# Performance work log

Measured on AMD Instinct MI355X. Metric: run time of the kernel, lower is better.

The kernel has to match this reference:

```python
import jax, jax.numpy as jnp
import numpy as np

EPS = 1e-6

def setup_inputs() -> dict:
    key = jax.random.key(0)
    S, U, D = 512, 32, 512
    dvecs = jax.random.normal(key, (S, U, D), dtype=jnp.float32)
    w = jnp.array([10.0], dtype=jnp.float32)
    b = jnp.array([-5.0], dtype=jnp.float32)
    return {"dvecs": dvecs, "w": w, "b": b}


def _ge2e_loss(dvecs, w, b):
    S, U, D = dvecs.shape
    # Full centroids [S, D]
    centroids = dvecs.mean(axis=1)
    # Leave-one-out centroids [S, U, D] (equivalent to the roll/unfold/mean trick)
    loo = (dvecs.sum(axis=1, keepdims=True) - dvecs) / (U - 1)
    # Norms, clamped like F.cosine_similarity eps
    dn = jnp.linalg.norm(dvecs, axis=-1)        # [S, U]
    cn = jnp.linalg.norm(centroids, axis=-1)    # [S]
    ln = jnp.linalg.norm(loo, axis=-1)          # [S, U]
    # Cosine sim of every utterance vs every speaker centroid: [S, U, S]
    sim_all = jnp.einsum('sud,jd->suj', dvecs, centroids) / jnp.maximum(dn[..., None] * cn[None, None, :], EPS)
    # Self-speaker column uses the leave-one-out centroid (index_copy in torch code)
    sim_self = jnp.einsum('sud,sud->su', dvecs, loo) / jnp.maximum(dn * ln, EPS)
    spk = jnp.arange(S)
    self_mask = spk[:, None, None] == spk[None, None, :]          # [S, 1, S] -> broadcasts to [S, U, S]
    sim = jnp.where(self_mask, sim_self[..., None], sim_all)
    logits = sim * w[0] + b[0]
    losses = -jax.nn.log_softmax(logits, axis=2)                  # [S, U, S]
    # Select losses[s, u, s] and sum (index_select of diagonal entries)
    return jnp.sum(jnp.where(self_mask, losses, 0.0))


def reference(dvecs, w, b):
    return _ge2e_loss(dvecs, w, b)
```

## Files before the change

### kernel.cpp

```cpp
#include <hip/hip_runtime.h>
#include <math.h>

#define NS 512
#define NU 32
#define ND 512
#define GEPS 1e-6f

typedef float f4 __attribute__((ext_vector_type(4)));
typedef _Float16 half8 __attribute__((ext_vector_type(8)));


__global__ __launch_bounds__(256) void prep_full(const float* __restrict__ dvecs,
                                                 _Float16* __restrict__ bpk,
                                                 float* __restrict__ cn2,
                                                 float* __restrict__ dn2,
                                                 _Float16* __restrict__ apk) {
    const int s = blockIdx.x, t = threadIdx.x;
    const int l = t & 63, wv = t >> 6, l15 = l & 15, lg = l >> 4;
    const float* base = dvecs + (size_t)s * NU * ND;
    __shared__ float red[4];

    const int d0 = t * 2;
    float sx = 0.f, sy = 0.f;
    #pragma unroll 4
    for (int u = 0; u < NU; ++u) {
        float2 v = *(const float2*)(base + u * ND + d0);
        sx += v.x; sy += v.y;
    }
    sx *= (1.0f / NU); sy *= (1.0f / NU);
    float c2 = sx * sx + sy * sy;
    #pragma unroll
    for (int m = 1; m < 64; m <<= 1) c2 += __shfl_xor(c2, m);
    if ((t & 63) == 0) red[t >> 6] = c2;

    {
        _Float16 hx = (_Float16)sx, hy = (_Float16)sy;
        _Float16 lx = (_Float16)(sx - (float)hx), ly = (_Float16)(sy - (float)hy);
        const int ct_g = s >> 4, cl15 = s & 15;
        const int tt = d0 >> 5, blg = (d0 >> 3) & 3, j = d0 & 7;
        size_t hbase = ((size_t)(ct_g * 16 + tt)) * 1024 + (blg * 16 + cl15) * 8 + j;
        unsigned hi2 = (unsigned)__builtin_bit_cast(unsigned short, hx)
                     | ((unsigned)__builtin_bit_cast(unsigned short, hy) << 16);
        unsigned lo2 = (unsigned)__builtin_bit_cast(unsigned short, lx)
                     | ((unsigned)__builtin_bit_cast(unsigned short, ly) << 16);
        *(unsigned*)(bpk + hbase)       = hi2;
        *(unsigned*)(bpk + hbase + 512) = lo2;
    }
    __syncthreads();
    if (t == 0) cn2[s] = red[0] + red[1] + red[2] + red[3];

    {
        const int u = t >> 3, jj = t & 7;
        const float* up = base + u * ND + jj * 4;
        float q = 0.f;
        #pragma unroll
        for (int i = 0; i < 16; ++i) {
            f4 v = *(const f4*)(up + i * 32);
            q += v[0]*v[0] + v[1]*v[1] + v[2]*v[2] + v[3]*v[3];
        }
        q += __shfl_xor(q, 1); q += __shfl_xor(q, 2); q += __shfl_xor(q, 4);
        if (jj == 0) dn2[s * NU + u] = q;
    }

    #pragma unroll
    for (int i = 0; i < 8; ++i) {
        const int idx = wv * 8 + i;
        const int rt = idx >> 4, tk = idx & 15;
        const int u = rt * 16 + l15, k = tk * 32 + lg * 8;
        const float* ap = base + (size_t)u * ND + k;
        f4 a0 = *(const f4*)ap;
        f4 a1 = *(const f4*)(ap + 4);
        half8 h, lo;
        #pragma unroll
        for (int i2 = 0; i2 < 4; ++i2) {
            _Float16 h0 = (_Float16)a0[i2];
            h[i2]     = h0; lo[i2]     = (_Float16)(a0[i2] - (float)h0);
            _Float16 h1 = (_Float16)a1[i2];
            h[4 + i2] = h1; lo[4 + i2] = (_Float16)(a1[i2] - (float)h1);
        }
        _Float16* cb = apk + ((size_t)(s * 2 + rt) * 16 + tk) * 1024 + l * 8;
        *(half8*)cb         = h;
        *(half8*)(cb + 512) = lo;
    }
}

__global__ __launch_bounds__(512, 4) void ge2e_full(const _Float16* __restrict__ apk,
                                                    const _Float16* __restrict__ bpk,
                                                    const float* __restrict__ cn2,
                                                    const float* __restrict__ dn2,
                                                    const float* __restrict__ wp,
                                                    const float* __restrict__ bp,
                                                    float* __restrict__ out) {
    const int s = blockIdx.x, tid = threadIdx.x;
    const int l = tid & 63, wv = tid >> 6;
    const int l15 = l & 15, lg = l >> 4;

    f4 acc[2][4];
    #pragma unroll
    for (int rt = 0; rt < 2; ++rt)
        #pragma unroll
        for (int ct = 0; ct < 4; ++ct) acc[rt][ct] = (f4){0.f, 0.f, 0.f, 0.f};

    const _Float16* Ab = apk + (size_t)s * 32 * 1024 + l * 8;
    const _Float16* Bb = bpk + (size_t)(wv * 4) * 16 * 1024 + l * 8;

    for (int t = 0; t < 16; ++t) {
        half8 bh[4], bl[4], ah[2], al[2];
        #pragma unroll
        for (int ct = 0; ct < 4; ++ct) {
            const _Float16* p = Bb + (size_t)(ct * 16 + t) * 1024;
            bh[ct] = *(const half8*)p;
            bl[ct] = *(const half8*)(p + 512);
        }
        #pragma unroll
        for (int rt = 0; rt < 2; ++rt) {
            const _Float16* p = Ab + (size_t)(rt * 16 + t) * 1024;
            ah[rt] = *(const half8*)p;
            al[rt] = *(const half8*)(p + 512);
        }
        #pragma unroll
        for (int ct = 0; ct < 4; ++ct)
            #pragma unroll
            for (int rt = 0; rt < 2; ++rt) {
                acc[rt][ct] = __builtin_amdgcn_mfma_f32_16x16x32_f16(ah[rt], bh[ct], acc[rt][ct], 0, 0, 0);
                acc[rt][ct] = __builtin_amdgcn_mfma_f32_16x16x32_f16(ah[rt], bl[ct], acc[rt][ct], 0, 0, 0);
                acc[rt][ct] = __builtin_amdgcn_mfma_f32_16x16x32_f16(al[rt], bh[ct], acc[rt][ct], 0, 0, 0);
                acc[rt][ct] = __builtin_amdgcn_mfma_f32_16x16x32_f16(al[rt], bl[ct], acc[rt][ct], 0, 0, 0);
            }
    }

    __shared__ float sDn2[32], sSelf[32], sMax[8][32], sSum[8][32], sRow[32];
    if (tid < 32) sDn2[tid] = dn2[s * NU + tid];
    __syncthreads();

    const float w = wp[0], bb = bp[0];
    const float cn2s = cn2[s];
    float dv[2][4];
    #pragma unroll
    for (int rt = 0; rt < 2; ++rt)
        #pragma unroll
        for (int r = 0; r < 4; ++r) dv[rt][r] = sDn2[rt * 16 + lg * 4 + r];

    const bool owner = (wv == (s >> 6)) && (l15 == (s & 15));
    const int  ctd   = (s >> 4) & 3;

    float dotc[2][4];
    #pragma unroll
    for (int ct = 0; ct < 4; ++ct)
        if (ct == ctd)
            #pragma unroll
            for (int rt = 0; rt < 2; ++rt)
                #pragma unroll
                for (int r = 0; r < 4; ++r) dotc[rt][r] = acc[rt][ct][r];

    #pragma unroll
    for (int ct = 0; ct < 4; ++ct) {
        const float cv = cn2[wv * 64 + ct * 16 + l15];
        #pragma unroll
        for (int rt = 0; rt < 2; ++rt)
            #pragma unroll
            for (int r = 0; r < 4; ++r)
                acc[rt][ct][r] = w * (acc[rt][ct][r] / fmaxf(sqrtf(dv[rt][r] * cv), GEPS)) + bb;
    }
    if (owner) {
        #pragma unroll
        for (int rt = 0; rt < 2; ++rt)
            #pragma unroll
            for (int r = 0; r < 4; ++r) {
                const float d2  = dv[rt][r];
                const float num = (float)NU * dotc[rt][r] - d2;
                const float X   = (float)(NU * NU) * cn2s - 2.0f * NU * dotc[rt][r] + d2;
                const float den = fmaxf(sqrtf(d2) * sqrtf(X), GEPS * (NU - 1));
                const float ls  = w * (num / den) + bb;
                #pragma unroll
                for (int ct = 0; ct < 4; ++ct)
                    if (ct == ctd) acc[rt][ct][r] = ls;
                sSelf[rt * 16 + lg * 4 + r] = ls;
            }
    }

    #pragma unroll
    for (int rt = 0; rt < 2; ++rt)
        #pragma unroll
        for (int r = 0; r < 4; ++r) {
            float mx = -INFINITY;
            #pragma unroll
            for (int ct = 0; ct < 4; ++ct) mx = fmaxf(mx, acc[rt][ct][r]);
            mx = fmaxf(mx, __shfl_xor(mx, 1)); mx = fmaxf(mx, __shfl_xor(mx, 2));
            mx = fmaxf(mx, __shfl_xor(mx, 4)); mx = fmaxf(mx, __shfl_xor(mx, 8));
            float se = 0.f;
            #pragma unroll
            for (int ct = 0; ct < 4; ++ct) se += expf(acc[rt][ct][r] - mx);
            se += __shfl_xor(se, 1); se += __shfl_xor(se, 2);
            se += __shfl_xor(se, 4); se += __shfl_xor(se, 8);
            if (l15 == 0) {
                sMax[wv][rt * 16 + lg * 4 + r] = mx;
                sSum[wv][rt * 16 + lg * 4 + r] = se;
            }
        }
    __syncthreads();

    if (tid < 32) {
        float M = -INFINITY;
        #pragma unroll
        for (int v = 0; v < 8; ++v) M = fmaxf(M, sMax[v][tid]);
        float S = 0.f;
        #pragma unroll
        for (int v = 0; v < 8; ++v) S += sSum[v][tid] * expf(sMax[v][tid] - M);
        sRow[tid] = logf(S) + M - sSelf[tid];
    }
    __syncthreads();
    if (tid == 0) {
        float tot = 0.f;
        #pragma unroll
        for (int u2 = 0; u2 < 32; ++u2) tot += sRow[u2];
        atomicAdd(out, tot);
    }
}


__global__ __launch_bounds__(256) void prep_fb(const float* __restrict__ dvecs,
                                               _Float16* __restrict__ bpk,
                                               float* __restrict__ cn2) {
    const int s = blockIdx.x, t = threadIdx.x;
    const float* base = dvecs + (size_t)s * NU * ND;
    const int d0 = t * 2;
    float sx = 0.f, sy = 0.f;
    for (int u = 0; u < NU; ++u) {
        float2 v = *(const float2*)(base + u * ND + d0);
        sx += v.x; sy += v.y;
    }
    sx *= (1.0f / NU); sy *= (1.0f / NU);
    float c2 = sx * sx + sy * sy;
    #pragma unroll
    for (int m = 1; m < 64; m <<= 1) c2 += __shfl_xor(c2, m);
    __shared__ float red[4];
    if ((t & 63) == 0) red[t >> 6] = c2;
    __syncthreads();
    if (t == 0) cn2[s] = red[0] + red[1] + red[2] + red[3];
    _Float16 hx = (_Float16)sx, hy = (_Float16)sy;
    _Float16 lx = (_Float16)(sx - (float)hx), ly = (_Float16)(sy - (float)hy);
    const int ct_g = s >> 4, l15 = s & 15;
    const int tt = d0 >> 5, lg = (d0 >> 3) & 3, j = d0 & 7;
    size_t hbase = ((size_t)(ct_g * 16 + tt)) * 1024 + (lg * 16 + l15) * 8 + j;
    unsigned hi2 = (unsigned)__builtin_bit_cast(unsigned short, hx)
                 | ((unsigned)__builtin_bit_cast(unsigned short, hy) << 16);
    unsigned lo2 = (unsigned)__builtin_bit_cast(unsigned short, lx)
                 | ((unsigned)__builtin_bit_cast(unsigned short, ly) << 16);
    *(unsigned*)(bpk + hbase)       = hi2;
    *(unsigned*)(bpk + hbase + 512) = lo2;
}

__global__ __launch_bounds__(512, 4) void ge2e_fb(const float* __restrict__ dvecs,
                                                  const _Float16* __restrict__ bpk,
                                                  const float* __restrict__ cn2,
                                                  const float* __restrict__ wp,
                                                  const float* __restrict__ bp,
                                                  float* __restrict__ out) {
    const int s = blockIdx.x, tid = threadIdx.x;
    const int l = tid & 63, wv = tid >> 6;
    const int l15 = l & 15, lg = l >> 4;
    f4 acc[2][4];
    #pragma unroll
    for (int rt = 0; rt < 2; ++rt)
        #pragma unroll
        for (int ct = 0; ct < 4; ++ct) acc[rt][ct] = (f4){0.f, 0.f, 0.f, 0.f};
    float dnp[2] = {0.f, 0.f};
    const float*    Ab0 = dvecs + (size_t)s * NU * ND + (size_t)l15 * ND + lg * 8;
    const _Float16* Bb  = bpk + (size_t)(wv * 4) * 16 * 1024 + l * 8;
    for (int t = 0; t < 16; ++t) {
        half8 bh[4], bl[4];
        #pragma unroll
        for (int ct = 0; ct < 4; ++ct) {
            const _Float16* p = Bb + (size_t)(ct * 16 + t) * 1024;
            bh[ct] = *(const half8*)p;
            bl[ct] = *(const half8*)(p + 512);
        }
        half8 ah[2], al[2];
        #pragma unroll
        for (int rt = 0; rt < 2; ++rt) {
            const float* ap = Ab0 + rt * 16 * ND + t * 32;
            f4 a0 = *(const f4*)ap, a1 = *(const f4*)(ap + 4);
            dnp[rt] += a0[0]*a0[0] + a0[1]*a0[1] + a0[2]*a0[2] + a0[3]*a0[3]
                     + a1[0]*a1[0] + a1[1]*a1[1] + a1[2]*a1[2] + a1[3]*a1[3];
            #pragma unroll
            for (int i = 0; i < 4; ++i) {
                _Float16 h0 = (_Float16)a0[i];
                ah[rt][i]     = h0; al[rt][i]     = (_Float16)(a0[i] - (float)h0);
                _Float16 h1 = (_Float16)a1[i];
                ah[rt][4 + i] = h1; al[rt][4 + i] = (_Float16)(a1[i] - (float)h1);
            }
        }
        #pragma unroll
        for (int ct = 0; ct < 4; ++ct)
            #pragma unroll
            for (int rt = 0; rt < 2; ++rt) {
                acc[rt][ct] = __builtin_amdgcn_mfma_f32_16x16x32_f16(ah[rt], bh[ct], acc[rt][ct], 0, 0, 0);
                acc[rt][ct] = __builtin_amdgcn_mfma_f32_16x16x32_f16(ah[rt], bl[ct], acc[rt][ct], 0, 0, 0);
                acc[rt][ct] = __builtin_amdgcn_mfma_f32_16x16x32_f16(al[rt], bh[ct], acc[rt][ct], 0, 0, 0);
                acc[rt][ct] = __builtin_amdgcn_mfma_f32_16x16x32_f16(al[rt], bl[ct], acc[rt][ct], 0, 0, 0);
            }
    }
    #pragma unroll
    for (int rt = 0; rt < 2; ++rt) {
        dnp[rt] += __shfl_xor(dnp[rt], 16);
        dnp[rt] += __shfl_xor(dnp[rt], 32);
    }
    __shared__ float sDn2[32], sSelf[32], sMax[8][32], sSum[8][32], sRow[32];
    if (wv == 0 && l < 16) { sDn2[l15] = dnp[0]; sDn2[16 + l15] = dnp[1]; }
    __syncthreads();
    const float w = wp[0], bb = bp[0];
    const float cn2s = cn2[s];
    float dv[2][4];
    #pragma unroll
    for (int rt = 0; rt < 2; ++rt)
        #pragma unroll
        for (int r = 0; r < 4; ++r) dv[rt][r] = sDn2[rt * 16 + lg * 4 + r];
    const bool owner = (wv == (s >> 6)) && (l15 == (s & 15));
    const int  ctd   = (s >> 4) & 3;
    float dotc[2][4];
    #pragma unroll
    for (int ct = 0; ct < 4; ++ct)
        if (ct == ctd)
            #pragma unroll
            for (int rt = 0; rt < 2; ++rt)
                #pragma unroll
                for (int r = 0; r < 4; ++r) dotc[rt][r] = acc[rt][ct][r];
    #pragma unroll
    for (int ct = 0; ct < 4; ++ct) {
        const float cv = cn2[wv * 64 + ct * 16 + l15];
        #pragma unroll
        for (int rt = 0; rt < 2; ++rt)
            #pragma unroll
            for (int r = 0; r < 4; ++r)
                acc[rt][ct][r] = w * (acc[rt][ct][r] / fmaxf(sqrtf(dv[rt][r] * cv), GEPS)) + bb;
    }
    if (owner) {
        #pragma unroll
        for (int rt = 0; rt < 2; ++rt)
            #pragma unroll
            for (int r = 0; r < 4; ++r) {
                const float d2  = dv[rt][r];
                const float num = (float)NU * dotc[rt][r] - d2;
                const float X   = (float)(NU * NU) * cn2s - 2.0f * NU * dotc[rt][r] + d2;
                const float den = fmaxf(sqrtf(d2) * sqrtf(X), GEPS * (NU - 1));
                const float ls  = w * (num / den) + bb;
                #pragma unroll
                for (int ct = 0; ct < 4; ++ct)
                    if (ct == ctd) acc[rt][ct][r] = ls;
                sSelf[rt * 16 + lg * 4 + r] = ls;
            }
    }
    #pragma unroll
    for (int rt = 0; rt < 2; ++rt)
        #pragma unroll
        for (int r = 0; r < 4; ++r) {
            float mx = -INFINITY;
            #pragma unroll
            for (int ct = 0; ct < 4; ++ct) mx = fmaxf(mx, acc[rt][ct][r]);
            mx = fmaxf(mx, __shfl_xor(mx, 1)); mx = fmaxf(mx, __shfl_xor(mx, 2));
            mx = fmaxf(mx, __shfl_xor(mx, 4)); mx = fmaxf(mx, __shfl_xor(mx, 8));
            float se = 0.f;
            #pragma unroll
            for (int ct = 0; ct < 4; ++ct) se += expf(acc[rt][ct][r] - mx);
            se += __shfl_xor(se, 1); se += __shfl_xor(se, 2);
            se += __shfl_xor(se, 4); se += __shfl_xor(se, 8);
            if (l15 == 0) {
                sMax[wv][rt * 16 + lg * 4 + r] = mx;
                sSum[wv][rt * 16 + lg * 4 + r] = se;
            }
        }
    __syncthreads();
    if (tid < 32) {
        float M = -INFINITY;
        #pragma unroll
        for (int v = 0; v < 8; ++v) M = fmaxf(M, sMax[v][tid]);
        float S = 0.f;
        #pragma unroll
        for (int v = 0; v < 8; ++v) S += sSum[v][tid] * expf(sMax[v][tid] - M);
        sRow[tid] = logf(S) + M - sSelf[tid];
    }
    __syncthreads();
    if (tid == 0) {
        float tot = 0.f;
        #pragma unroll
        for (int u2 = 0; u2 < 32; ++u2) tot += sRow[u2];
        atomicAdd(out, tot);
    }
}

extern "C" void kernel_launch(void* const* d_in, const int* in_sizes, int n_in,
                              void* d_out, int out_size, void* d_ws, size_t ws_size,
                              hipStream_t stream) {
    const float* dvecs = (const float*)d_in[0];
    const float* w     = (const float*)d_in[1];
    const float* b     = (const float*)d_in[2];
    float* out = (float*)d_out;

    const size_t bpk_b = (size_t)32 * 16 * 1024 * sizeof(_Float16);
    const size_t cn2_b = (size_t)NS * sizeof(float);
    const size_t dn2_b = (size_t)NS * NU * sizeof(float);
    const size_t apk_b = (size_t)NS * 2 * 16 * 1024 * sizeof(_Float16);
    const size_t need  = bpk_b + cn2_b + dn2_b + apk_b;

    char* p = (char*)d_ws;
    _Float16* bpk = (_Float16*)p;                 p += bpk_b;
    float*    cn2 = (float*)p;                    p += cn2_b;
    float*    dn2 = (float*)p;                    p += dn2_b;
    _Float16* apk = (_Float16*)p;

    hipMemsetAsync(d_out, 0, sizeof(float), stream);
    if (ws_size >= need) {
        prep_full<<<NS, 256, 0, stream>>>(dvecs, bpk, cn2, dn2, apk);
        ge2e_full<<<NS, 512, 0, stream>>>(apk, bpk, cn2, dn2, w, b, out);
    } else {
        prep_fb<<<NS, 256, 0, stream>>>(dvecs, bpk, cn2);
        ge2e_fb<<<NS, 512, 0, stream>>>(dvecs, bpk, cn2, w, b, out);
    }
}
```

Before: 128.4 us.

## Fuse prep passes into one read and tune GEMM loop scheduling

The prep kernel now reads each dvecs row once and derives the fp16 hi/lo split, the squared norms and the partial centroid sums from that single read. The sums are reduced through lane shuffles and shared memory, where the old code made three separate passes over global memory. The main GEMM kernel marks the wave index as uniform, fully unrolls the k-loop with scalar base pointers, and raises wave priority around the MFMA block. The extra shuffles and shared-memory traffic in prep, and the higher register pressure from full unrolling, are the costs.

```diff
diff --git a/kernel.cpp b/kernel.cpp
--- a/kernel.cpp
+++ b/kernel.cpp
@@ -16,72 +16,80 @@
                                                  float* __restrict__ dn2,
                                                  _Float16* __restrict__ apk) {
     const int s = blockIdx.x, t = threadIdx.x;
-    const int l = t & 63, wv = t >> 6, l15 = l & 15, lg = l >> 4;
+    const int l = t & 63, w = t >> 6, l15 = l & 15, lg = l >> 4;
+    const int rt = w >> 1, tkh = (w & 1) * 8;
     const float* base = dvecs + (size_t)s * NU * ND;
+
+    __shared__ float centp[2][512];
+    __shared__ float dn2p[4][16];
     __shared__ float red[4];
 
-    const int d0 = t * 2;
-    float sx = 0.f, sy = 0.f;
-    #pragma unroll 4
-    for (int u = 0; u < NU; ++u) {
-        float2 v = *(const float2*)(base + u * ND + d0);
-        sx += v.x; sy += v.y;
-    }
-    sx *= (1.0f / NU); sy *= (1.0f / NU);
-    float c2 = sx * sx + sy * sy;
-    #pragma unroll
-    for (int m = 1; m < 64; m <<= 1) c2 += __shfl_xor(c2, m);
-    if ((t & 63) == 0) red[t >> 6] = c2;
-
-    {
-        _Float16 hx = (_Float16)sx, hy = (_Float16)sy;
-        _Float16 lx = (_Float16)(sx - (float)hx), ly = (_Float16)(sy - (float)hy);
-        const int ct_g = s >> 4, cl15 = s & 15;
-        const int tt = d0 >> 5, blg = (d0 >> 3) & 3, j = d0 & 7;
-        size_t hbase = ((size_t)(ct_g * 16 + tt)) * 1024 + (blg * 16 + cl15) * 8 + j;
-        unsigned hi2 = (unsigned)__builtin_bit_cast(unsigned short, hx)
-                     | ((unsigned)__builtin_bit_cast(unsigned short, hy) << 16);
-        unsigned lo2 = (unsigned)__builtin_bit_cast(unsigned short, lx)
-                     | ((unsigned)__builtin_bit_cast(unsigned short, ly) << 16);
-        *(unsigned*)(bpk + hbase)       = hi2;
-        *(unsigned*)(bpk + hbase + 512) = lo2;
-    }
-    __syncthreads();
-    if (t == 0) cn2[s] = red[0] + red[1] + red[2] + red[3];
-
-    {
-        const int u = t >> 3, jj = t & 7;
-        const float* up = base + u * ND + jj * 4;
-        float q = 0.f;
-        #pragma unroll
-        for (int i = 0; i < 16; ++i) {
-            f4 v = *(const f4*)(up + i * 32);
-            q += v[0]*v[0] + v[1]*v[1] + v[2]*v[2] + v[3]*v[3];
-        }
-        q += __shfl_xor(q, 1); q += __shfl_xor(q, 2); q += __shfl_xor(q, 4);
-        if (jj == 0) dn2[s * NU + u] = q;
-    }
+    const int u = rt * 16 + l15;
+    const float* rowp = base + (size_t)u * ND;
+    float q = 0.f;
 
     #pragma unroll
     for (int i = 0; i < 8; ++i) {
-        const int idx = wv * 8 + i;
-        const int rt = idx >> 4, tk = idx & 15;
-        const int u = rt * 16 + l15, k = tk * 32 + lg * 8;
-        const float* ap = base + (size_t)u * ND + k;
-        f4 a0 = *(const f4*)ap;
-        f4 a1 = *(const f4*)(ap + 4);
+        const int tk = tkh + i;
+        const int k0 = tk * 32 + lg * 8;
+        f4 a0 = *(const f4*)(rowp + k0);
+        f4 a1 = *(const f4*)(rowp + k0 + 4);
+        q += a0[0]*a0[0] + a0[1]*a0[1] + a0[2]*a0[2] + a0[3]*a0[3]
+           + a1[0]*a1[0] + a1[1]*a1[1] + a1[2]*a1[2] + a1[3]*a1[3];
         half8 h, lo;
         #pragma unroll
-        for (int i2 = 0; i2 < 4; ++i2) {
-            _Float16 h0 = (_Float16)a0[i2];
-            h[i2]     = h0; lo[i2]     = (_Float16)(a0[i2] - (float)h0);
-            _Float16 h1 = (_Float16)a1[i2];
-            h[4 + i2] = h1; lo[4 + i2] = (_Float16)(a1[i2] - (float)h1);
+        for (int c = 0; c < 4; ++c) {
+            _Float16 h0 = (_Float16)a0[c];
+            h[c]     = h0; lo[c]     = (_Float16)(a0[c] - (float)h0);
+            _Float16 h1 = (_Float16)a1[c];
+            h[4 + c] = h1; lo[4 + c] = (_Float16)(a1[c] - (float)h1);
         }
         _Float16* cb = apk + ((size_t)(s * 2 + rt) * 16 + tk) * 1024 + l * 8;
         *(half8*)cb         = h;
         *(half8*)(cb + 512) = lo;
-    }
+        f4 s0 = a0, s1 = a1;
+        #pragma unroll
+        for (int m = 1; m <= 8; m <<= 1) {
+            #pragma unroll
+            for (int c = 0; c < 4; ++c) {
+                s0[c] += __shfl_xor(s0[c], m);
+                s1[c] += __shfl_xor(s1[c], m);
+            }
+        }
+        if (l15 == 0) {
+            *(f4*)&centp[rt][k0]     = s0;
+            *(f4*)&centp[rt][k0 + 4] = s1;
+        }
+    }
+    q += __shfl_xor(q, 16);
+    q += __shfl_xor(q, 32);
+    if (lg == 0) dn2p[w][l15] = q;
+    __syncthreads();
+
+    if (t < 32)
+        dn2[s * NU + t] = dn2p[(t >> 4) * 2][t & 15] + dn2p[(t >> 4) * 2 + 1][t & 15];
+
+    const int d0 = t * 2;
+    float cx = (centp[0][d0]     + centp[1][d0])     * (1.0f / NU);
+    float cy = (centp[0][d0 + 1] + centp[1][d0 + 1]) * (1.0f / NU);
+    float c2 = cx * cx + cy * cy;
+    #pragma unroll
+    for (int m = 1; m < 64; m <<= 1) c2 += __shfl_xor(c2, m);
+    if ((t & 63) == 0) red[t >> 6] = c2;
+    __syncthreads();
+    if (t == 0) cn2[s] = red[0] + red[1] + red[2] + red[3];
+
+    _Float16 hx = (_Float16)cx, hy = (_Float16)cy;
+    _Float16 lx = (_Float16)(cx - (float)hx), ly = (_Float16)(cy - (float)hy);
+    const int ct_g = s >> 4, cl15 = s & 15;
+    const int tt = d0 >> 5, blg = (d0 >> 3) & 3, j = d0 & 7;
+    size_t hbase = ((size_t)(ct_g * 16 + tt)) * 1024 + (blg * 16 + cl15) * 8 + j;
+    unsigned hi2 = (unsigned)__builtin_bit_cast(unsigned short, hx)
+                 | ((unsigned)__builtin_bit_cast(unsigned short, hy) << 16);
+    unsigned lo2 = (unsigned)__builtin_bit_cast(unsigned short, lx)
+                 | ((unsigned)__builtin_bit_cast(unsigned short, ly) << 16);
+    *(unsigned*)(bpk + hbase)       = hi2;
+    *(unsigned*)(bpk + hbase + 512) = lo2;
 }
 
 __global__ __launch_bounds__(512, 4) void ge2e_full(const _Float16* __restrict__ apk,
@@ -92,7 +100,8 @@
                                                     const float* __restrict__ bp,
                                                     float* __restrict__ out) {
     const int s = blockIdx.x, tid = threadIdx.x;
-    const int l = tid & 63, wv = tid >> 6;
+    const int l = tid & 63;
+    const int wv = __builtin_amdgcn_readfirstlane(tid >> 6);
     const int l15 = l & 15, lg = l >> 4;
 
     f4 acc[2][4];
@@ -101,23 +110,26 @@
         #pragma unroll
         for (int ct = 0; ct < 4; ++ct) acc[rt][ct] = (f4){0.f, 0.f, 0.f, 0.f};
 
-    const _Float16* Ab = apk + (size_t)s * 32 * 1024 + l * 8;
-    const _Float16* Bb = bpk + (size_t)(wv * 4) * 16 * 1024 + l * 8;
-
+    const _Float16* Au = apk + (size_t)s * 32 * 1024;
+    const _Float16* Bu = bpk + (size_t)(wv * 4) * 16 * 1024;
+    const int voff = l * 8;
+
+    #pragma unroll
     for (int t = 0; t < 16; ++t) {
-        half8 bh[4], bl[4], ah[2], al[2];
+        half8 ah[2], al[2], bh[4], bl[4];
+        #pragma unroll
+        for (int rt = 0; rt < 2; ++rt) {
+            const _Float16* p = Au + (rt * 16 + t) * 1024 + voff;
+            ah[rt] = *(const half8*)p;
+            al[rt] = *(const half8*)(p + 512);
+        }
         #pragma unroll
         for (int ct = 0; ct < 4; ++ct) {
-            const _Float16* p = Bb + (size_t)(ct * 16 + t) * 1024;
+            const _Float16* p = Bu + (ct * 16 + t) * 1024 + voff;
             bh[ct] = *(const half8*)p;
             bl[ct] = *(const half8*)(p + 512);
         }
-        #pragma unroll
-        for (int rt = 0; rt < 2; ++rt) {
-            const _Float16* p = Ab + (size_t)(rt * 16 + t) * 1024;
-            ah[rt] = *(const half8*)p;
-            al[rt] = *(const half8*)(p + 512);
-        }
+        __builtin_amdgcn_s_setprio(1);
         #pragma unroll
         for (int ct = 0; ct < 4; ++ct)
             #pragma unroll
@@ -127,6 +139,7 @@
                 acc[rt][ct] = __builtin_amdgcn_mfma_f32_16x16x32_f16(al[rt], bh[ct], acc[rt][ct], 0, 0, 0);
                 acc[rt][ct] = __builtin_amdgcn_mfma_f32_16x16x32_f16(al[rt], bl[ct], acc[rt][ct], 0, 0, 0);
             }
+        __builtin_amdgcn_s_setprio(0);
     }
 
     __shared__ float sDn2[32], sSelf[32], sMax[8][32], sSum[8][32], sRow[32];
```

Measured after the change: 126.7 us. Within noise of the previous version (-1.3%).
